# Performance work log

Measured on AMD Instinct MI355X. Metric: run time of the kernel, lower is better.

The kernel has to match this reference:

```python
import jax, jax.numpy as jnp
import numpy as np

N_QUBITS = 8
INPUT_DIM = 32
HIDDEN_DIM = 8  # must equal N_QUBITS (gate outputs multiply cell state elementwise)
BATCH = 1024
SEQ_LEN = 64


def _cnot_perm(n):
    """Composite basis-state permutation for CNOT chain (0,1)..(n-2,n-1) then ring (n-1,0).
    Wire 0 is the most-significant bit. Returns gather indices: new[k] = old[perm[k]]."""
    idx = np.arange(2 ** n)
    gates = [(w, w + 1) for w in range(n - 1)] + [(n - 1, 0)]
    for c, t in reversed(gates):  # compose g1(g2(...gm(k)))
        sc, st = n - 1 - c, n - 1 - t
        idx = idx ^ (((idx >> sc) & 1) << st)
    return jnp.asarray(idx)


def _z_signs(n):
    """signs[k, i] = +1 if bit i of basis state k is 0 else -1 (PauliZ eigenvalue)."""
    k = np.arange(2 ** n)[:, None]
    w = (n - 1 - np.arange(n))[None, :]
    return jnp.asarray((1 - 2 * ((k >> w) & 1)).astype(np.float32))


_PERM = _cnot_perm(N_QUBITS)
_SIGNS = _z_signs(N_QUBITS)


def _qlayer(y, theta):
    """Exact statevector sim of: RX(y_i) encoder + trainable RX(theta_i) per wire,
    CNOT chain + ring, MeasureAll(PauliZ).
    RX gates on |0> give a product state with real/imaginary amplitude split, and
    CNOTs are phase-free basis permutations, so PauliZ expectations depend only on
    basis probabilities: p0=cos^2(a/2), p1=sin^2(a/2) with a = y + theta."""
    a = 0.5 * (y + theta)                                    # (B, n)
    p = jnp.stack([jnp.cos(a) ** 2, jnp.sin(a) ** 2], -1)    # (B, n, 2)
    probs = p[:, 0]                                          # (B, 2)
    for w in range(1, p.shape[1]):                           # small fixed loop over wires
        probs = (probs[:, :, None] * p[:, w, None, :]).reshape(probs.shape[0], -1)
    probs = probs[:, _PERM]                                  # apply CNOT permutation
    return probs @ _SIGNS                                    # (B, n) <Z_i>


def setup_inputs() -> dict:
    key = jax.random.key(0)
    ks = jax.random.split(key, 13)
    d = INPUT_DIM + HIDDEN_DIM
    s = 1.0 / np.sqrt(d)
    inp = {"inputs": jax.random.normal(ks[0], (BATCH, SEQ_LEN, INPUT_DIM), jnp.float32)}
    for j, nm in enumerate(["forget", "input", "update", "output"]):
        inp[f"W_{nm}"] = jax.random.uniform(ks[1 + 3 * j], (N_QUBITS, d), jnp.float32, -s, s)
        inp[f"b_{nm}"] = jax.random.uniform(ks[2 + 3 * j], (N_QUBITS,), jnp.float32, -s, s)
        inp[f"theta_{nm}"] = jax.random.uniform(ks[3 + 3 * j], (N_QUBITS,), jnp.float32, -np.pi, np.pi)
    return inp


def reference(inputs, W_forget, b_forget, theta_forget,
              W_input, b_input, theta_input,
              W_update, b_update, theta_update,
              W_output, b_output, theta_output):
    B = inputs.shape[0]
    hx0 = jnp.zeros((B, HIDDEN_DIM), inputs.dtype)
    cx0 = jnp.zeros((B, HIDDEN_DIM), inputs.dtype)

    def step(carry, x):
        hx, cx = carry
        comb = jnp.concatenate([x, hx], axis=-1)
        f = jax.nn.sigmoid(_qlayer(comb @ W_forget.T + b_forget, theta_forget))
        i = jax.nn.sigmoid(_qlayer(comb @ W_input.T + b_input, theta_input))
        g = jnp.tanh(_qlayer(comb @ W_update.T + b_update, theta_update))
        o = jax.nn.sigmoid(_qlayer(comb @ W_output.T + b_output, theta_output))
        cx2 = f * cx + i * g
        hx2 = o * jnp.tanh(cx2)
        return (hx2, cx2), hx2

    (hx, cx), ys = jax.lax.scan(step, (hx0, cx0), jnp.swapaxes(inputs, 0, 1))
    out_seq = jnp.swapaxes(ys, 0, 1)  # (B, T, hidden)
    return out_seq, hx, cx
```

## Files before the change

kernel.cpp:

```cpp
#include <hip/hip_runtime.h>

#define B_TOT 1024
#define SEQ 64
#define IND 32
#define HID 8
#define BPB 4

typedef __attribute__((ext_vector_type(2))) float f2;

template<int CTRL>
__device__ __forceinline__ float dppf(float v) {
    return __int_as_float(__builtin_amdgcn_update_dpp(
        0, __float_as_int(v), CTRL, 0xF, 0xF, true));
}
template<int CTRL>
__device__ __forceinline__ f2 dpp2(f2 v) {
    f2 r;
    r.x = dppf<CTRL>(v.x);
    r.y = dppf<CTRL>(v.y);
    return r;
}

__global__ __launch_bounds__(512, 1) void qlstm_kernel(
    const float* __restrict__ xin,
    const float* __restrict__ Wf, const float* __restrict__ bf, const float* __restrict__ thf,
    const float* __restrict__ Wi, const float* __restrict__ bi, const float* __restrict__ thi,
    const float* __restrict__ Wu, const float* __restrict__ bu, const float* __restrict__ thu,
    const float* __restrict__ Wo, const float* __restrict__ bo, const float* __restrict__ tho,
    float* __restrict__ out)
{
    __shared__ float zs[BPB][SEQ + 1][33];

    const int tid = threadIdx.x;

    {
        const int sub = tid >> 8;
        const int idx = tid & 255;
        const int bl  = idx >> 6;
        const int t   = idx & 63;
        const int gb  = blockIdx.x * BPB + bl;
        const float4* xp = (const float4*)(xin + ((size_t)gb * SEQ + t) * IND);
        float4 x4[8];
        #pragma unroll
        for (int k = 0; k < 8; ++k) x4[k] = xp[k];

        #pragma unroll
        for (int j = 0; j < 16; ++j) {
            const int row = j & 7;
            const float* W = sub ? (j < 8 ? Wu : Wo) : (j < 8 ? Wf : Wi);
            const float* B = sub ? (j < 8 ? bu : bo) : (j < 8 ? bf : bi);
            const float* T = sub ? (j < 8 ? thu : tho) : (j < 8 ? thf : thi);
            const float4* wr = (const float4*)(W + row * 40);
            float a0 = B[row] + T[row], a1 = 0.f, a2 = 0.f, a3 = 0.f;
            #pragma unroll
            for (int k = 0; k < 8; ++k) {
                float4 w4 = wr[k];
                a0 = fmaf(w4.x, x4[k].x, a0);
                a1 = fmaf(w4.y, x4[k].y, a1);
                a2 = fmaf(w4.z, x4[k].z, a2);
                a3 = fmaf(w4.w, x4[k].w, a3);
            }
            zs[bl][t][(sub << 4) | j] = (a0 + a1) + (a2 + a3);
        }
    }

    __syncthreads();
    if (tid >= 64) return;

    const int lane = tid;
    const int b    = lane >> 4;
    const int l16  = lane & 15;
    const int p    = l16 >> 3;
    const int r    = l16 & 7;
    const int gb   = blockIdx.x * BPB + b;
    const bool isP0 = (p == 0);
    const bool r0   = (r == 0);
    const bool ge1 = (r >= 1), ge2 = (r >= 2), ge4 = (r >= 4);

    const int m[8] = {0, 1, 2, 3, 7, 6, 5, 4};
    const float* WA = p ? Wi : Wf;
    const float* WB = p ? Wo : Wu;
    f2 wh[8];
    #pragma unroll
    for (int k = 0; k < 8; ++k) {
        wh[k].x = WA[r * 40 + 32 + (r ^ m[k])];
        wh[k].y = WB[r * 40 + 32 + (r ^ m[k])];
    }
    const f2 esAB = {-1.0f, p ? -1.0f : 2.0f};
    const f2 cMul = { 1.0f, p ?  1.0f : -2.0f};
    const f2 cAdd = { 0.0f, p ?  0.0f :  1.0f};
    const f2 one2 = { 1.0f, 1.0f};

    float* obase = out + (size_t)gb * (SEQ * HID);

    float cx = 0.f, hlast = 0.f;
    float hv[8] = {0.f, 0.f, 0.f, 0.f, 0.f, 0.f, 0.f, 0.f};
    f2 z = { zs[b][0][l16], zs[b][0][l16 + 16] };

    #pragma unroll 2
    for (int t = 0; t < SEQ; ++t) {
        const int tn = (t + 1) & 63;
        f2 zn = { zs[b][tn][l16], zs[b][tn][l16 + 16] };

        f2 y0 = z, y1 = {0.f, 0.f};
        #pragma unroll
        for (int k = 0; k < 4; ++k) {
            y0 += wh[2 * k]     * (f2){hv[2 * k],     hv[2 * k]};
            y1 += wh[2 * k + 1] * (f2){hv[2 * k + 1], hv[2 * k + 1]};
        }
        f2 y = y0 + y1;

        f2 a = y * 0.15915494309189535f;
        a.x = __builtin_amdgcn_fractf(a.x);
        a.y = __builtin_amdgcn_fractf(a.y);
        f2 c;
        c.x = __builtin_amdgcn_cosf(a.x);
        c.y = __builtin_amdgcn_cosf(a.y);

        f2 mm = { r0 ? 1.0f : c.x, r0 ? 1.0f : c.y };
        mm *= dpp2<0xB1>(mm);
        mm *= dpp2<0x4E>(mm);
        mm *= dpp2<0x141>(mm);

        f2 v = c, tt;
        tt = dpp2<0x111>(v); v *= ge1 ? tt : one2;
        tt = dpp2<0x112>(v); v *= ge2 ? tt : one2;
        tt = dpp2<0x114>(v); v *= ge4 ? tt : one2;

        f2 q = { r0 ? mm.x : v.x, r0 ? mm.y : v.y };

        f2 arg = q * esAB;
        f2 e;
        e.x = __expf(arg.x);
        e.y = __expf(arg.y);
        f2 s = e + one2;
        f2 rr;
        rr.x = __builtin_amdgcn_rcpf(s.x);
        rr.y = __builtin_amdgcn_rcpf(s.y);
        f2 act = rr * cMul + cAdd;

        float oA = dppf<0x128>(act.x);
        float oB = dppf<0x128>(act.y);
        float fv = isP0 ? act.x : oA;
        float iv = isP0 ? oA : act.x;
        float gv = isP0 ? act.y : oB;
        float ov = isP0 ? oB : act.y;

        cx = fmaf(fv, cx, iv * gv);
        float e2 = __expf(2.0f * cx);
        float th = fmaf(-2.0f, __builtin_amdgcn_rcpf(1.0f + e2), 1.0f);
        float h  = ov * th;
        hlast = h;

        if (isP0) obase[t * HID + r] = h;

        hv[0] = h;
        hv[1] = dppf<0xB1>(h);
        hv[2] = dppf<0x4E>(hv[0]);
        hv[3] = dppf<0x4E>(hv[1]);
        hv[4] = dppf<0x141>(hv[0]);
        hv[5] = dppf<0x141>(hv[1]);
        hv[6] = dppf<0x141>(hv[2]);
        hv[7] = dppf<0x141>(hv[3]);

        z = zn;
    }

    if (isP0) {
        const size_t hx_off = (size_t)B_TOT * SEQ * HID;
        out[hx_off + (size_t)gb * HID + r] = hlast;
        out[hx_off + (size_t)B_TOT * HID + (size_t)gb * HID + r] = cx;
    }
}

extern "C" void kernel_launch(void* const* d_in, const int* in_sizes, int n_in,
                              void* d_out, int out_size, void* d_ws, size_t ws_size,
                              hipStream_t stream) {
    qlstm_kernel<<<256, 512, 0, stream>>>(
        (const float*)d_in[0],
        (const float*)d_in[1],  (const float*)d_in[2],  (const float*)d_in[3],
        (const float*)d_in[4],  (const float*)d_in[5],  (const float*)d_in[6],
        (const float*)d_in[7],  (const float*)d_in[8],  (const float*)d_in[9],
        (const float*)d_in[10], (const float*)d_in[11], (const float*)d_in[12],
        (float*)d_out);
}
```

Baseline: 29.31 us.

## Process eight batches per block with one lane computing all four gates

Each lane now handles all four gates (f,u,i,o) for one qubit, so a 64-lane wave covers eight batch rows instead of four. The grid shrinks to 128 blocks of 512 threads. The 1/(2*pi) scale is folded into the precomputed z and recurrent weights, which removes the per-step multiply and fract. The z tile is stored as rotated float4 rows and prefetched two steps ahead. The point is to halve the number of serial recurrence waves and remove the cross-half DPP exchange, at the cost of more per-lane ALU work per step, fewer blocks than CUs, and no fract range reduction before cos.

```diff
diff --git a/kernel.cpp b/kernel.cpp
--- a/kernel.cpp
+++ b/kernel.cpp
@@ -4,7 +4,8 @@
 #define SEQ 64
 #define IND 32
 #define HID 8
-#define BPB 4
+#define BPB 8
+#define INV2PI 0.15915494309189535f
 
 typedef __attribute__((ext_vector_type(2))) float f2;
 
@@ -15,10 +16,7 @@
 }
 template<int CTRL>
 __device__ __forceinline__ f2 dpp2(f2 v) {
-    f2 r;
-    r.x = dppf<CTRL>(v.x);
-    r.y = dppf<CTRL>(v.y);
-    return r;
+    f2 r; r.x = dppf<CTRL>(v.x); r.y = dppf<CTRL>(v.y); return r;
 }
 
 __global__ __launch_bounds__(512, 1) void qlstm_kernel(
@@ -29,130 +27,123 @@
     const float* __restrict__ Wo, const float* __restrict__ bo, const float* __restrict__ tho,
     float* __restrict__ out)
 {
-    __shared__ float zs[BPB][SEQ + 1][33];
+    __shared__ float zs[BPB * SEQ * 32];
 
     const int tid = threadIdx.x;
 
     {
-        const int sub = tid >> 8;
-        const int idx = tid & 255;
-        const int bl  = idx >> 6;
-        const int t   = idx & 63;
-        const int gb  = blockIdx.x * BPB + bl;
+        const int b = tid >> 6;
+        const int t = tid & 63;
+        const int gb = blockIdx.x * BPB + b;
         const float4* xp = (const float4*)(xin + ((size_t)gb * SEQ + t) * IND);
         float4 x4[8];
         #pragma unroll
         for (int k = 0; k < 8; ++k) x4[k] = xp[k];
 
+        const float* Ws[4] = {Wf, Wu, Wi, Wo};
+        const float* Bs[4] = {bf, bu, bi, bo};
+        const float* Ts[4] = {thf, thu, thi, tho};
+        float zv[32];
         #pragma unroll
-        for (int j = 0; j < 16; ++j) {
-            const int row = j & 7;
-            const float* W = sub ? (j < 8 ? Wu : Wo) : (j < 8 ? Wf : Wi);
-            const float* B = sub ? (j < 8 ? bu : bo) : (j < 8 ? bf : bi);
-            const float* T = sub ? (j < 8 ? thu : tho) : (j < 8 ? thf : thi);
-            const float4* wr = (const float4*)(W + row * 40);
-            float a0 = B[row] + T[row], a1 = 0.f, a2 = 0.f, a3 = 0.f;
+        for (int g = 0; g < 4; ++g) {
             #pragma unroll
-            for (int k = 0; k < 8; ++k) {
-                float4 w4 = wr[k];
-                a0 = fmaf(w4.x, x4[k].x, a0);
-                a1 = fmaf(w4.y, x4[k].y, a1);
-                a2 = fmaf(w4.z, x4[k].z, a2);
-                a3 = fmaf(w4.w, x4[k].w, a3);
+            for (int row = 0; row < 8; ++row) {
+                const float4* wr = (const float4*)(Ws[g] + row * 40);
+                float a0 = Bs[g][row] + Ts[g][row], a1 = 0.f, a2 = 0.f, a3 = 0.f;
+                #pragma unroll
+                for (int k = 0; k < 8; ++k) {
+                    float4 w4 = wr[k];
+                    a0 = fmaf(w4.x, x4[k].x, a0);
+                    a1 = fmaf(w4.y, x4[k].y, a1);
+                    a2 = fmaf(w4.z, x4[k].z, a2);
+                    a3 = fmaf(w4.w, x4[k].w, a3);
+                }
+                zv[row * 4 + g] = ((a0 + a1) + (a2 + a3)) * INV2PI;
             }
-            zs[bl][t][(sub << 4) | j] = (a0 + a1) + (a2 + a3);
         }
+        float4* zrow = (float4*)(zs + (b * SEQ + t) * 32);
+        const float4* zvp = (const float4*)zv;
+        #pragma unroll
+        for (int r4 = 0; r4 < 8; ++r4) zrow[(r4 + t) & 7] = zvp[r4];
     }
 
     __syncthreads();
     if (tid >= 64) return;
 
-    const int lane = tid;
-    const int b    = lane >> 4;
-    const int l16  = lane & 15;
-    const int p    = l16 >> 3;
-    const int r    = l16 & 7;
-    const int gb   = blockIdx.x * BPB + b;
-    const bool isP0 = (p == 0);
-    const bool r0   = (r == 0);
+    const int l = tid;
+    const int b = l >> 3;
+    const int r = l & 7;
+    const int gb = blockIdx.x * BPB + b;
+    const bool r0  = (r == 0);
     const bool ge1 = (r >= 1), ge2 = (r >= 2), ge4 = (r >= 4);
+    const f2 one2 = {1.0f, 1.0f};
 
     const int m[8] = {0, 1, 2, 3, 7, 6, 5, 4};
-    const float* WA = p ? Wi : Wf;
-    const float* WB = p ? Wo : Wu;
-    f2 wh[8];
+    f2 wh0[8], wh1[8];
     #pragma unroll
     for (int k = 0; k < 8; ++k) {
-        wh[k].x = WA[r * 40 + 32 + (r ^ m[k])];
-        wh[k].y = WB[r * 40 + 32 + (r ^ m[k])];
+        const int j = r * 40 + 32 + (r ^ m[k]);
+        wh0[k] = (f2){Wf[j] * INV2PI, Wu[j] * INV2PI};
+        wh1[k] = (f2){Wi[j] * INV2PI, Wo[j] * INV2PI};
     }
-    const f2 esAB = {-1.0f, p ? -1.0f : 2.0f};
-    const f2 cMul = { 1.0f, p ?  1.0f : -2.0f};
-    const f2 cAdd = { 0.0f, p ?  0.0f :  1.0f};
-    const f2 one2 = { 1.0f, 1.0f};
 
     float* obase = out + (size_t)gb * (SEQ * HID);
+    const float4* zp = (const float4*)zs;
+    const int zb = b * SEQ;
 
-    float cx = 0.f, hlast = 0.f;
+    float cx = 0.f, h = 0.f;
     float hv[8] = {0.f, 0.f, 0.f, 0.f, 0.f, 0.f, 0.f, 0.f};
-    f2 z = { zs[b][0][l16], zs[b][0][l16 + 16] };
+    float4 zc = zp[(zb + 0) * 8 + (r & 7)];
+    float4 z1 = zp[(zb + 1) * 8 + ((r + 1) & 7)];
 
-    #pragma unroll 2
+    #pragma unroll 4
     for (int t = 0; t < SEQ; ++t) {
-        const int tn = (t + 1) & 63;
-        f2 zn = { zs[b][tn][l16], zs[b][tn][l16 + 16] };
+        const int tt = (t + 2) & 63;
+        float4 z2 = zp[(zb + tt) * 8 + ((r + tt) & 7)];
 
-        f2 y0 = z, y1 = {0.f, 0.f};
+        f2 y0a = (f2){zc.x, zc.y}, y0b = (f2){0.f, 0.f};
+        f2 y1a = (f2){zc.z, zc.w}, y1b = (f2){0.f, 0.f};
         #pragma unroll
         for (int k = 0; k < 4; ++k) {
-            y0 += wh[2 * k]     * (f2){hv[2 * k],     hv[2 * k]};
-            y1 += wh[2 * k + 1] * (f2){hv[2 * k + 1], hv[2 * k + 1]};
+            f2 e0 = (f2){hv[2 * k],     hv[2 * k]};
+            f2 e1 = (f2){hv[2 * k + 1], hv[2 * k + 1]};
+            y0a += wh0[2 * k] * e0;  y0b += wh0[2 * k + 1] * e1;
+            y1a += wh1[2 * k] * e0;  y1b += wh1[2 * k + 1] * e1;
         }
-        f2 y = y0 + y1;
+        f2 y0 = y0a + y0b, y1 = y1a + y1b;
 
-        f2 a = y * 0.15915494309189535f;
-        a.x = __builtin_amdgcn_fractf(a.x);
-        a.y = __builtin_amdgcn_fractf(a.y);
-        f2 c;
-        c.x = __builtin_amdgcn_cosf(a.x);
-        c.y = __builtin_amdgcn_cosf(a.y);
+        f2 c0, c1;
+        c0.x = __builtin_amdgcn_cosf(y0.x); c0.y = __builtin_amdgcn_cosf(y0.y);
+        c1.x = __builtin_amdgcn_cosf(y1.x); c1.y = __builtin_amdgcn_cosf(y1.y);
 
-        f2 mm = { r0 ? 1.0f : c.x, r0 ? 1.0f : c.y };
-        mm *= dpp2<0xB1>(mm);
-        mm *= dpp2<0x4E>(mm);
-        mm *= dpp2<0x141>(mm);
+        f2 m0 = r0 ? one2 : c0, m1 = r0 ? one2 : c1;
+        m0 *= dpp2<0xB1>(m0);  m1 *= dpp2<0xB1>(m1);
+        m0 *= dpp2<0x4E>(m0);  m1 *= dpp2<0x4E>(m1);
+        m0 *= dpp2<0x141>(m0); m1 *= dpp2<0x141>(m1);
+        f2 v0 = c0, v1 = c1, tt0, tt1;
+        tt0 = dpp2<0x111>(v0); tt1 = dpp2<0x111>(v1);
+        v0 *= ge1 ? tt0 : one2;  v1 *= ge1 ? tt1 : one2;
+        tt0 = dpp2<0x112>(v0); tt1 = dpp2<0x112>(v1);
+        v0 *= ge2 ? tt0 : one2;  v1 *= ge2 ? tt1 : one2;
+        tt0 = dpp2<0x114>(v0); tt1 = dpp2<0x114>(v1);
+        v0 *= ge4 ? tt0 : one2;  v1 *= ge4 ? tt1 : one2;
+        f2 q0 = r0 ? m0 : v0, q1 = r0 ? m1 : v1;
 
-        f2 v = c, tt;
-        tt = dpp2<0x111>(v); v *= ge1 ? tt : one2;
-        tt = dpp2<0x112>(v); v *= ge2 ? tt : one2;
-        tt = dpp2<0x114>(v); v *= ge4 ? tt : one2;
+        float ef = __expf(-q0.x);
+        float eg = __expf(q0.y + q0.y);
+        float ei = __expf(-q1.x);
+        float eo = __expf(-q1.y);
+        float f_ = __builtin_amdgcn_rcpf(1.0f + ef);
+        float g_ = fmaf(-2.0f, __builtin_amdgcn_rcpf(1.0f + eg), 1.0f);
+        float i_ = __builtin_amdgcn_rcpf(1.0f + ei);
+        float o_ = __builtin_amdgcn_rcpf(1.0f + eo);
 
-        f2 q = { r0 ? mm.x : v.x, r0 ? mm.y : v.y };
+        cx = fmaf(f_, cx, i_ * g_);
+        float e2 = __expf(cx + cx);
+        float th = fmaf(-2.0f, __builtin_amdgcn_rcpf(1.0f + e2), 1.0f);
+        h = o_ * th;
 
-        f2 arg = q * esAB;
-        f2 e;
-        e.x = __expf(arg.x);
-        e.y = __expf(arg.y);
-        f2 s = e + one2;
-        f2 rr;
-        rr.x = __builtin_amdgcn_rcpf(s.x);
-        rr.y = __builtin_amdgcn_rcpf(s.y);
-        f2 act = rr * cMul + cAdd;
-
-        float oA = dppf<0x128>(act.x);
-        float oB = dppf<0x128>(act.y);
-        float fv = isP0 ? act.x : oA;
-        float iv = isP0 ? oA : act.x;
-        float gv = isP0 ? act.y : oB;
-        float ov = isP0 ? oB : act.y;
-
-        cx = fmaf(fv, cx, iv * gv);
-        float e2 = __expf(2.0f * cx);
-        float th = fmaf(-2.0f, __builtin_amdgcn_rcpf(1.0f + e2), 1.0f);
-        float h  = ov * th;
-        hlast = h;
-
-        if (isP0) obase[t * HID + r] = h;
+        obase[t * HID + r] = h;
 
         hv[0] = h;
         hv[1] = dppf<0xB1>(h);
@@ -163,20 +154,18 @@
         hv[6] = dppf<0x141>(hv[2]);
         hv[7] = dppf<0x141>(hv[3]);
 
-        z = zn;
+        zc = z1; z1 = z2;
     }
 
-    if (isP0) {
-        const size_t hx_off = (size_t)B_TOT * SEQ * HID;
-        out[hx_off + (size_t)gb * HID + r] = hlast;
-        out[hx_off + (size_t)B_TOT * HID + (size_t)gb * HID + r] = cx;
-    }
+    const size_t hxoff = (size_t)B_TOT * SEQ * HID;
+    out[hxoff + (size_t)gb * HID + r] = h;
+    out[hxoff + (size_t)B_TOT * HID + (size_t)gb * HID + r] = cx;
 }
 
 extern "C" void kernel_launch(void* const* d_in, const int* in_sizes, int n_in,
                               void* d_out, int out_size, void* d_ws, size_t ws_size,
                               hipStream_t stream) {
-    qlstm_kernel<<<256, 512, 0, stream>>>(
+    qlstm_kernel<<<128, 512, 0, stream>>>(
         (const float*)d_in[0],
         (const float*)d_in[1],  (const float*)d_in[2],  (const float*)d_in[3],
         (const float*)d_in[4],  (const float*)d_in[5],  (const float*)d_in[6],
```

Result: slower. 30.46 us (+3.9%).

## Relayout recurrent lanes, fold 2π scaling, and use polynomial sigmoid/tanh approximations

Applied to the files above, without the earlier changes.

Lanes in the serial recurrence are remapped so each (batch, row) pair gets two adjacent lanes holding the gate pairs, and the z staging layout in LDS is changed to match. The 1/(2π) factor is folded into the precomputed z and recurrent weights, so the fract and multiply before cos are dropped. The exp+rcp sigmoid/tanh are replaced by odd polynomial and Padé rational approximations, and DPP with a bound_ctrl-style default of 1.0 removes the selects in the prefix product. The aim is a shorter serial dependency chain per timestep. The risks are accuracy loss from the approximations, especially the tanh of cx when its magnitude grows, and removing fract assumes the cos builtin handles the unreduced range.

```diff
diff --git a/kernel.cpp b/kernel.cpp
--- a/kernel.cpp
+++ b/kernel.cpp
@@ -5,20 +5,28 @@
 #define IND 32
 #define HID 8
 #define BPB 4
+#define ZSTRIDE 34
+#define INV2PI 0.15915494309189535f
 
 typedef __attribute__((ext_vector_type(2))) float f2;
 
 template<int CTRL>
-__device__ __forceinline__ float dppf(float v) {
+__device__ __forceinline__ float dppx(float v) {
     return __int_as_float(__builtin_amdgcn_update_dpp(
         0, __float_as_int(v), CTRL, 0xF, 0xF, true));
 }
 template<int CTRL>
-__device__ __forceinline__ f2 dpp2(f2 v) {
-    f2 r;
-    r.x = dppf<CTRL>(v.x);
-    r.y = dppf<CTRL>(v.y);
-    return r;
+__device__ __forceinline__ f2 dppx2(f2 v) {
+    f2 r; r.x = dppx<CTRL>(v.x); r.y = dppx<CTRL>(v.y); return r;
+}
+template<int CTRL>
+__device__ __forceinline__ float dppone(float v) {
+    return __int_as_float(__builtin_amdgcn_update_dpp(
+        0x3f800000, __float_as_int(v), CTRL, 0xF, 0xF, false));
+}
+template<int CTRL>
+__device__ __forceinline__ f2 dppone2(f2 v) {
+    f2 r; r.x = dppone<CTRL>(v.x); r.y = dppone<CTRL>(v.y); return r;
 }
 
 __global__ __launch_bounds__(512, 1) void qlstm_kernel(
@@ -29,7 +37,7 @@
     const float* __restrict__ Wo, const float* __restrict__ bo, const float* __restrict__ tho,
     float* __restrict__ out)
 {
-    __shared__ float zs[BPB][SEQ + 1][33];
+    __shared__ float zs[BPB * 65 * ZSTRIDE];
 
     const int tid = threadIdx.x;
 
@@ -44,9 +52,11 @@
         #pragma unroll
         for (int k = 0; k < 8; ++k) x4[k] = xp[k];
 
+        float* zrow = zs + (bl * 65 + t) * ZSTRIDE;
         #pragma unroll
         for (int j = 0; j < 16; ++j) {
-            const int row = j & 7;
+            const int row  = j & 7;
+            const int gidx = ((j >> 3) << 1) | sub;
             const float* W = sub ? (j < 8 ? Wu : Wo) : (j < 8 ? Wf : Wi);
             const float* B = sub ? (j < 8 ? bu : bo) : (j < 8 ? bf : bi);
             const float* T = sub ? (j < 8 ? thu : tho) : (j < 8 ? thf : thi);
@@ -60,117 +70,117 @@
                 a2 = fmaf(w4.z, x4[k].z, a2);
                 a3 = fmaf(w4.w, x4[k].w, a3);
             }
-            zs[bl][t][(sub << 4) | j] = (a0 + a1) + (a2 + a3);
+            zrow[row * 4 + gidx] = ((a0 + a1) + (a2 + a3)) * INV2PI;
         }
     }
 
     __syncthreads();
     if (tid >= 64) return;
 
-    const int lane = tid;
-    const int b    = lane >> 4;
-    const int l16  = lane & 15;
-    const int p    = l16 >> 3;
-    const int r    = l16 & 7;
-    const int gb   = blockIdx.x * BPB + b;
-    const bool isP0 = (p == 0);
-    const bool r0   = (r == 0);
-    const bool ge1 = (r >= 1), ge2 = (r >= 2), ge4 = (r >= 4);
+    const int l  = tid;
+    const int b  = l >> 4;
+    const int r  = (l >> 1) & 7;
+    const int c  = l & 1;
+    const int gb = blockIdx.x * BPB + b;
+    const bool r0 = (r == 0);
+    const bool cb = (c == 1);
 
-    const int m[8] = {0, 1, 2, 3, 7, 6, 5, 4};
-    const float* WA = p ? Wi : Wf;
-    const float* WB = p ? Wo : Wu;
+    const float* WX = c ? Wi : Wf;
+    const float* WY = c ? Wo : Wu;
     f2 wh[8];
     #pragma unroll
     for (int k = 0; k < 8; ++k) {
-        wh[k].x = WA[r * 40 + 32 + (r ^ m[k])];
-        wh[k].y = WB[r * 40 + 32 + (r ^ m[k])];
+        const int j = r * 40 + 32 + (r ^ k);
+        wh[k] = (f2){WX[j] * INV2PI, WY[j] * INV2PI};
     }
-    const f2 esAB = {-1.0f, p ? -1.0f : 2.0f};
-    const f2 cMul = { 1.0f, p ?  1.0f : -2.0f};
-    const f2 cAdd = { 0.0f, p ?  0.0f :  1.0f};
-    const f2 one2 = { 1.0f, 1.0f};
 
-    float* obase = out + (size_t)gb * (SEQ * HID);
+    float* obase = out + (size_t)gb * (SEQ * HID) + r;
+    const float* zbase = zs + (b * 65) * ZSTRIDE + r * 4 + c * 2;
 
-    float cx = 0.f, hlast = 0.f;
-    float hv[8] = {0.f, 0.f, 0.f, 0.f, 0.f, 0.f, 0.f, 0.f};
-    f2 z = { zs[b][0][l16], zs[b][0][l16 + 16] };
+    float cx = 0.f, h = 0.f;
+    float hv0 = 0.f, hv1 = 0.f, hv2 = 0.f, hv3 = 0.f,
+          hv4 = 0.f, hv5 = 0.f, hv6 = 0.f, hv7 = 0.f;
+    f2 zc = *(const f2*)(zbase);
+    f2 z1 = *(const f2*)(zbase + ZSTRIDE);
+
+    const f2 P5 = { 0.00208333333f,  0.00208333333f};
+    const f2 P3 = {-0.0208333333f,  -0.0208333333f};
+    const f2 P1 = { 0.25f, 0.25f};
+    const f2 PH = { 0.5f,  0.5f};
+    const f2 one2 = {1.0f, 1.0f};
 
     #pragma unroll 2
     for (int t = 0; t < SEQ; ++t) {
-        const int tn = (t + 1) & 63;
-        f2 zn = { zs[b][tn][l16], zs[b][tn][l16 + 16] };
+        f2 z2 = *(const f2*)(zbase + ((t + 2) & 63) * ZSTRIDE);
 
-        f2 y0 = z, y1 = {0.f, 0.f};
-        #pragma unroll
-        for (int k = 0; k < 4; ++k) {
-            y0 += wh[2 * k]     * (f2){hv[2 * k],     hv[2 * k]};
-            y1 += wh[2 * k + 1] * (f2){hv[2 * k + 1], hv[2 * k + 1]};
-        }
+        f2 y0 = zc, y1;
+        y0 += wh[0] * (f2){hv0, hv0};
+        y1  = wh[4] * (f2){hv4, hv4};
+        y0 += wh[1] * (f2){hv1, hv1};
+        y1 += wh[5] * (f2){hv5, hv5};
+        y0 += wh[2] * (f2){hv2, hv2};
+        y1 += wh[6] * (f2){hv6, hv6};
+        y0 += wh[3] * (f2){hv3, hv3};
+        y1 += wh[7] * (f2){hv7, hv7};
         f2 y = y0 + y1;
 
-        f2 a = y * 0.15915494309189535f;
-        a.x = __builtin_amdgcn_fractf(a.x);
-        a.y = __builtin_amdgcn_fractf(a.y);
-        f2 c;
-        c.x = __builtin_amdgcn_cosf(a.x);
-        c.y = __builtin_amdgcn_cosf(a.y);
+        f2 cc;
+        cc.x = __builtin_amdgcn_cosf(y.x);
+        cc.y = __builtin_amdgcn_cosf(y.y);
 
-        f2 mm = { r0 ? 1.0f : c.x, r0 ? 1.0f : c.y };
-        mm *= dpp2<0xB1>(mm);
-        mm *= dpp2<0x4E>(mm);
-        mm *= dpp2<0x141>(mm);
-
-        f2 v = c, tt;
-        tt = dpp2<0x111>(v); v *= ge1 ? tt : one2;
-        tt = dpp2<0x112>(v); v *= ge2 ? tt : one2;
-        tt = dpp2<0x114>(v); v *= ge4 ? tt : one2;
-
+        f2 v = cc;
+        v *= dppone2<0x112>(v);
+        v *= dppone2<0x114>(v);
+        v *= dppone2<0x118>(v);
+        f2 mm = { r0 ? 1.0f : cc.x, r0 ? 1.0f : cc.y };
+        mm *= dppx2<0x122>(mm);
+        mm *= dppx2<0x124>(mm);
+        mm *= dppx2<0x128>(mm);
         f2 q = { r0 ? mm.x : v.x, r0 ? mm.y : v.y };
 
-        f2 arg = q * esAB;
-        f2 e;
-        e.x = __expf(arg.x);
-        e.y = __expf(arg.y);
-        f2 s = e + one2;
-        f2 rr;
-        rr.x = __builtin_amdgcn_rcpf(s.x);
-        rr.y = __builtin_amdgcn_rcpf(s.y);
-        f2 act = rr * cMul + cAdd;
+        f2 s  = q * q;
+        f2 p  = s * P5 + P3;
+        p     = s * p + P1;
+        f2 sg = q * p + PH;
+        float sy  = s.y;
+        float n54 = fmaf(sy + 105.0f, sy, 945.0f);
+        float d54 = fmaf(fmaf(15.0f, sy, 420.0f), sy, 945.0f);
+        float t54 = q.y * n54 * __builtin_amdgcn_rcpf(d54);
+        float ax = sg.x;
+        float ay = cb ? sg.y : t54;
 
-        float oA = dppf<0x128>(act.x);
-        float oB = dppf<0x128>(act.y);
-        float fv = isP0 ? act.x : oA;
-        float iv = isP0 ? oA : act.x;
-        float gv = isP0 ? act.y : oB;
-        float ov = isP0 ? oB : act.y;
+        float bx = dppx<0xB1>(ax);
+        float by = dppx<0xB1>(ay);
+        float f_ = cb ? bx : ax;
+        float i_ = cb ? ax : bx;
+        float g_ = cb ? by : ay;
+        float o_ = cb ? ay : by;
 
-        cx = fmaf(fv, cx, iv * gv);
-        float e2 = __expf(2.0f * cx);
-        float th = fmaf(-2.0f, __builtin_amdgcn_rcpf(1.0f + e2), 1.0f);
-        float h  = ov * th;
-        hlast = h;
+        cx = fmaf(f_, cx, i_ * g_);
+        float sc  = cx * cx;
+        float n76 = fmaf(fmaf(sc + 378.0f, sc, 17325.0f), sc, 135135.0f);
+        float d76 = fmaf(fmaf(fmaf(28.0f, sc, 3150.0f), sc, 62370.0f), sc, 135135.0f);
+        float th  = cx * n76 * __builtin_amdgcn_rcpf(d76);
+        h = o_ * th;
 
-        if (isP0) obase[t * HID + r] = h;
+        obase[t * HID] = h;
 
-        hv[0] = h;
-        hv[1] = dppf<0xB1>(h);
-        hv[2] = dppf<0x4E>(hv[0]);
-        hv[3] = dppf<0x4E>(hv[1]);
-        hv[4] = dppf<0x141>(hv[0]);
-        hv[5] = dppf<0x141>(hv[1]);
-        hv[6] = dppf<0x141>(hv[2]);
-        hv[7] = dppf<0x141>(hv[3]);
+        hv0 = h;
+        hv1 = dppx<0x4E>(h);
+        float a7 = dppx<0x141>(h);
+        hv2 = dppx<0x1B>(a7);
+        hv3 = dppx<0x4E>(hv2);
+        hv4 = dppx<0x128>(h);
+        hv5 = dppx<0x128>(hv1);
+        hv6 = dppx<0x128>(hv2);
+        hv7 = dppx<0x128>(hv3);
 
-        z = zn;
+        zc = z1; z1 = z2;
     }
 
-    if (isP0) {
-        const size_t hx_off = (size_t)B_TOT * SEQ * HID;
-        out[hx_off + (size_t)gb * HID + r] = hlast;
-        out[hx_off + (size_t)B_TOT * HID + (size_t)gb * HID + r] = cx;
-    }
+    const size_t hxoff = (size_t)B_TOT * SEQ * HID;
+    out[hxoff + (size_t)gb * HID + r] = h;
+    out[hxoff + (size_t)B_TOT * HID + (size_t)gb * HID + r] = cx;
 }
 
 extern "C" void kernel_launch(void* const* d_in, const int* in_sizes, int n_in,
```

Result: no change. 29.24 us (-0.3%).
